# Optimization experiments

Hardware: AMD Instinct MI355X
Metric: run time of the kernel (lower is better)

## Reference

```python
import jax, jax.numpy as jnp
import numpy as np

N_NODES = 100000
N_EDGES = 1600000
D = 128
N_GRAPHS = 128
N_LAYERS = 3


def setup_inputs() -> dict:
    key = jax.random.key(0)
    ks = jax.random.split(key, 3 + 4 * N_LAYERS)
    x = jax.random.normal(ks[0], (N_NODES, D), dtype=jnp.float32)
    edge_index = jax.random.randint(ks[1], (2, N_EDGES), 0, N_NODES, dtype=jnp.int64)
    batch = jnp.sort(jax.random.randint(ks[2], (N_NODES,), 0, N_GRAPHS, dtype=jnp.int64))
    inp = {"x": x, "edge_index": edge_index, "batch": batch}
    scale = 1.0 / np.sqrt(D)
    for l in range(N_LAYERS):
        inp[f"W1_{l}"] = jax.random.normal(ks[3 + 4 * l], (D, D), dtype=jnp.float32) * scale
        inp[f"b1_{l}"] = jnp.zeros((D,), dtype=jnp.float32)
        inp[f"W2_{l}"] = jax.random.normal(ks[4 + 4 * l], (D, D), dtype=jnp.float32) * scale
        inp[f"b2_{l}"] = jnp.zeros((D,), dtype=jnp.float32)
    return inp


def _gin_conv(x, edge_index, W1, b1, W2, b2):
    # GINConv with eps=0: out = MLP(x + sum_{j in N(i)} x_j)
    msgs = x[edge_index[0]]                                   # [E, D] gather
    agg = jax.ops.segment_sum(msgs, edge_index[1], num_segments=N_NODES)
    h = x + agg
    h = jax.nn.relu(h @ W1 + b1)
    return h @ W2 + b2


def reference(x, edge_index, batch,
              W1_0, b1_0, W2_0, b2_0,
              W1_1, b1_1, W2_1, b2_1,
              W1_2, b1_2, W2_2, b2_2):
    params = [(W1_0, b1_0, W2_0, b2_0), (W1_1, b1_1, W2_1, b2_1), (W1_2, b1_2, W2_2, b2_2)]
    h = x
    for l in range(N_LAYERS - 1):
        h = _gin_conv(h, edge_index, *params[l])
        h = jax.nn.relu(h)  # act; dropout with drop_ratio=0 is identity
    node_emb = _gin_conv(h, edge_index, *params[-1])  # JK='last'
    # global_mean_pool
    sums = jax.ops.segment_sum(node_emb, batch, num_segments=N_GRAPHS)
    counts = jax.ops.segment_sum(jnp.ones((N_NODES, 1), node_emb.dtype), batch, num_segments=N_GRAPHS)
    graph_emb = sums / jnp.maximum(counts, 1.0)
    return graph_emb
```

## Files before the change

kernel.cpp:

```cpp
#include <hip/hip_runtime.h>
#include <hip/hip_bf16.h>

#define N_NODES 100000
#define N_PAD   100032
#define N_EDGES 1600000
#define DIM 128
#define N_GRAPHS 128
#define NBKT 98
#define BSTRIDE 18432
#define TILES (N_PAD / 16)
#define GRID_MLP 1563
#define POOL_BLKS ((N_NODES + 127) / 128)
#define B1_BATCH 4096
#define B1_GRID ((N_EDGES + B1_BATCH - 1) / B1_BATCH)

typedef unsigned short u16;
typedef unsigned int u32;
typedef __attribute__((ext_vector_type(8))) short bf16x8;
typedef __attribute__((ext_vector_type(4))) float f32x4;

#define MFMA(A, B, C) __builtin_amdgcn_mfma_f32_16x16x32_bf16(A, B, C, 0, 0, 0)

__device__ __forceinline__ u16 f2bf(float x) {
    u32 u = __float_as_uint(x);
    u = (u + 0x7FFFu + ((u >> 16) & 1u)) >> 16;
    return (u16)u;
}
__device__ __forceinline__ float bf2f(u16 u) {
    return __uint_as_float(((u32)u) << 16);
}

__global__ __launch_bounds__(256) void bucket1_kernel(const int* __restrict__ src,
                                                      const int* __restrict__ dst,
                                                      u32* __restrict__ cursorB,
                                                      u32* __restrict__ pairs) {
    __shared__ int lh[NBKT];
    __shared__ u32 lbase[NBKT];
    int t = threadIdx.x;
    if (t < NBKT) lh[t] = 0;
    __syncthreads();
    int e0 = blockIdx.x * B1_BATCH;
    int d[16], s[16], rk[16];
#pragma unroll
    for (int k = 0; k < 16; ++k) {
        int e = e0 + t + k * 256;
        if (e < N_EDGES) {
            d[k] = dst[e];
            s[k] = src[e];
            rk[k] = atomicAdd(&lh[d[k] >> 10], 1);
        }
    }
    __syncthreads();
    if (t < NBKT) lbase[t] = atomicAdd(&cursorB[t], (u32)lh[t]) + (u32)(t * BSTRIDE);
    __syncthreads();
#pragma unroll
    for (int k = 0; k < 16; ++k) {
        int e = e0 + t + k * 256;
        if (e < N_EDGES) {
            u32 pos = lbase[d[k] >> 10] + (u32)rk[k];
            pairs[pos] = ((u32)(d[k] & 1023) << 22) | (u32)s[k];
        }
    }
}

__global__ __launch_bounds__(1024) void bucket2_kernel(const u32* __restrict__ cursorB,
                                                       const u32* __restrict__ pairs,
                                                       int* __restrict__ row_ptr,
                                                       int* __restrict__ csr) {
    __shared__ int lh[1024];
    __shared__ int rc[1024];
    __shared__ int bs[128];
    int b = blockIdx.x, t = threadIdx.x;

    if (t < 128) bs[t] = (t < NBKT) ? (int)cursorB[t] : 0;
    __syncthreads();
    for (int off = 1; off < 128; off <<= 1) {
        int v = (t < 128 && t >= off) ? bs[t - off] : 0;
        __syncthreads();
        if (t < 128) bs[t] += v;
        __syncthreads();
    }
    int cnt = (int)cursorB[b];
    int bbase = (b == 0) ? 0 : bs[b - 1];

    lh[t] = 0;
    __syncthreads();
    const u32* pb = pairs + (size_t)b * BSTRIDE;
    for (int i = t; i < cnt; i += 1024) atomicAdd(&lh[__builtin_nontemporal_load(pb + i) >> 22], 1);
    __syncthreads();

    int own = lh[t];
    for (int off = 1; off < 1024; off <<= 1) {
        int v = (t >= off) ? lh[t - off] : 0;
        __syncthreads();
        lh[t] += v;
        __syncthreads();
    }
    int excl = lh[t] - own;
    int node = b * 1024 + t;
    if (node < N_NODES) row_ptr[node] = bbase + excl;
    if (b == 0 && t == 0) row_ptr[N_NODES] = N_EDGES;
    rc[t] = bbase + excl;
    __syncthreads();

    for (int i = t; i < cnt; i += 1024) {
        u32 p = __builtin_nontemporal_load(pb + i);
        int pos = atomicAdd(&rc[p >> 22], 1);
        csr[pos] = (int)(p & 0x3FFFFFu);
    }
}

__global__ __launch_bounds__(256) void xprep_kernel(const float* __restrict__ x,
                                                    u16* __restrict__ hb) {
    int i = blockIdx.x * 256 + threadIdx.x;
    if (i < N_NODES * 32) {
        float4 v = ((const float4*)x)[i];
        ushort4 o;
        o.x = f2bf(v.x); o.y = f2bf(v.y); o.z = f2bf(v.z); o.w = f2bf(v.w);
        ((ushort4*)hb)[i] = o;
    }
}

__global__ __launch_bounds__(256) void agg_kernel(const u16* __restrict__ hb,
                                                  const int* __restrict__ rp,
                                                  const int* __restrict__ csr,
                                                  u16* __restrict__ Ah) {
    int node = (blockIdx.x * 256 + threadIdx.x) >> 5;
    int l = threadIdx.x & 31;
    if (node >= N_NODES) return;
    const ushort4* h4 = (const ushort4*)hb;
    ushort4 sv = h4[(size_t)node * 32 + l];
    float a0 = bf2f(sv.x), a1 = bf2f(sv.y), a2 = bf2f(sv.z), a3 = bf2f(sv.w);
    int s = rp[node], e = rp[node + 1];
    int i = s;
    for (; i + 8 <= e; i += 8) {
        ushort4 v0 = h4[(size_t)csr[i + 0] * 32 + l];
        ushort4 v1 = h4[(size_t)csr[i + 1] * 32 + l];
        ushort4 v2 = h4[(size_t)csr[i + 2] * 32 + l];
        ushort4 v3 = h4[(size_t)csr[i + 3] * 32 + l];
        ushort4 v4 = h4[(size_t)csr[i + 4] * 32 + l];
        ushort4 v5 = h4[(size_t)csr[i + 5] * 32 + l];
        ushort4 v6 = h4[(size_t)csr[i + 6] * 32 + l];
        ushort4 v7 = h4[(size_t)csr[i + 7] * 32 + l];
        a0 += ((bf2f(v0.x) + bf2f(v1.x)) + (bf2f(v2.x) + bf2f(v3.x))) +
              ((bf2f(v4.x) + bf2f(v5.x)) + (bf2f(v6.x) + bf2f(v7.x)));
        a1 += ((bf2f(v0.y) + bf2f(v1.y)) + (bf2f(v2.y) + bf2f(v3.y))) +
              ((bf2f(v4.y) + bf2f(v5.y)) + (bf2f(v6.y) + bf2f(v7.y)));
        a2 += ((bf2f(v0.z) + bf2f(v1.z)) + (bf2f(v2.z) + bf2f(v3.z))) +
              ((bf2f(v4.z) + bf2f(v5.z)) + (bf2f(v6.z) + bf2f(v7.z)));
        a3 += ((bf2f(v0.w) + bf2f(v1.w)) + (bf2f(v2.w) + bf2f(v3.w))) +
              ((bf2f(v4.w) + bf2f(v5.w)) + (bf2f(v6.w) + bf2f(v7.w)));
    }
    for (; i < e; ++i) {
        ushort4 v = h4[(size_t)csr[i] * 32 + l];
        a0 += bf2f(v.x); a1 += bf2f(v.y); a2 += bf2f(v.z); a3 += bf2f(v.w);
    }
    ushort4 hv;
    hv.x = f2bf(a0); hv.y = f2bf(a1); hv.z = f2bf(a2); hv.w = f2bf(a3);
    *(ushort4*)(Ah + (size_t)node * 128 + l * 4) = hv;
}

struct WPrepArgs {
    const float* w[6];
    u16* buf[6];
};
__global__ __launch_bounds__(256) void wprep_kernel(WPrepArgs p) {
    int m = blockIdx.y;
    int idx = blockIdx.x * 256 + threadIdx.x;
    int n = idx >> 7, k = idx & 127;
    float v = p.w[m][k * 128 + n];
    u16 hi = f2bf(v);
    p.buf[m][idx] = hi;
    p.buf[m][idx + 16384] = f2bf(v - bf2f(hi));
}

#define HS 136
__global__ __launch_bounds__(256, 2) void fused_mlp(const u16* __restrict__ Ah,
                                                    const u16* __restrict__ W1,
                                                    const float* __restrict__ b1,
                                                    const u16* __restrict__ W2,
                                                    const float* __restrict__ b2,
                                                    u16* __restrict__ Cb, int relu) {
    __shared__ u16 Hh[64 * HS];
    __shared__ u16 Hl[64 * HS];
    int tid = threadIdx.x;
    int lane = tid & 63, wave = tid >> 6;
    int m16 = lane & 15, quad = lane >> 4;
    int colBase = wave * 32;

    float b1v[2][4], b2v[2][4];
#pragma unroll
    for (int nt = 0; nt < 2; ++nt)
#pragma unroll
        for (int rg = 0; rg < 4; ++rg) {
            int col = colBase + nt * 16 + quad * 4 + rg;
            b1v[nt][rg] = b1[col];
            b2v[nt][rg] = b2[col];
        }

    f32x4 z = {0.f, 0.f, 0.f, 0.f};
    bf16x8 aH[4][4];

    int t0 = blockIdx.x * 4;
    if (t0 >= TILES) return;
#pragma unroll
    for (int p = 0; p < 4; ++p) {
        const u16* ah = Ah + (size_t)((t0 + p) * 16 + m16) * 128 + quad * 8;
#pragma unroll
        for (int kb = 0; kb < 4; ++kb)
            aH[p][kb] = *(const bf16x8*)(ah + kb * 32);
    }

    bf16x8 W1H[2][4], W1L[2][4];
#pragma unroll
    for (int nt = 0; nt < 2; ++nt) {
        int n = colBase + nt * 16 + m16;
#pragma unroll
        for (int kb = 0; kb < 4; ++kb) {
            int off = n * 128 + kb * 32 + quad * 8;
            W1H[nt][kb] = *(const bf16x8*)(W1 + off);
            W1L[nt][kb] = *(const bf16x8*)(W1 + off + 16384);
        }
    }

    f32x4 acc[4][2];
#pragma unroll
    for (int p = 0; p < 4; ++p) { acc[p][0] = z; acc[p][1] = z; }

#pragma unroll
    for (int kb = 0; kb < 4; ++kb) {
#pragma unroll
        for (int p = 0; p < 4; ++p) {
            acc[p][0] = MFMA(W1H[0][kb], aH[p][kb], acc[p][0]);
            acc[p][1] = MFMA(W1H[1][kb], aH[p][kb], acc[p][1]);
            acc[p][0] = MFMA(W1L[0][kb], aH[p][kb], acc[p][0]);
            acc[p][1] = MFMA(W1L[1][kb], aH[p][kb], acc[p][1]);
        }
    }

#pragma unroll
    for (int p = 0; p < 4; ++p) {
#pragma unroll
        for (int nt = 0; nt < 2; ++nt) {
            ushort4 hv, lv;
#pragma unroll
            for (int rg = 0; rg < 4; ++rg) {
                float v = fmaxf(acc[p][nt][rg] + b1v[nt][rg], 0.f);
                u16 hi = f2bf(v);
                ((u16*)&hv)[rg] = hi;
                ((u16*)&lv)[rg] = f2bf(v - bf2f(hi));
            }
            int off = (p * 16 + m16) * HS + colBase + nt * 16 + quad * 4;
            *(ushort4*)&Hh[off] = hv;
            *(ushort4*)&Hl[off] = lv;
        }
    }
    __syncthreads();

    bf16x8 W2H[2][4], W2L[2][4];
#pragma unroll
    for (int nt = 0; nt < 2; ++nt) {
        int n = colBase + nt * 16 + m16;
#pragma unroll
        for (int kb = 0; kb < 4; ++kb) {
            int off = n * 128 + kb * 32 + quad * 8;
            W2H[nt][kb] = *(const bf16x8*)(W2 + off);
            W2L[nt][kb] = *(const bf16x8*)(W2 + off + 16384);
        }
    }

    f32x4 acc2[4][2];
#pragma unroll
    for (int p = 0; p < 4; ++p) { acc2[p][0] = z; acc2[p][1] = z; }
#pragma unroll
    for (int kb = 0; kb < 4; ++kb) {
#pragma unroll
        for (int p = 0; p < 4; ++p) {
            int off = (p * 16 + m16) * HS + kb * 32 + quad * 8;
            bf16x8 hH = *(const bf16x8*)(&Hh[off]);
            bf16x8 hL = *(const bf16x8*)(&Hl[off]);
            acc2[p][0] = MFMA(W2H[0][kb], hH, acc2[p][0]);
            acc2[p][1] = MFMA(W2H[1][kb], hH, acc2[p][1]);
            acc2[p][0] = MFMA(W2H[0][kb], hL, acc2[p][0]);
            acc2[p][1] = MFMA(W2H[1][kb], hL, acc2[p][1]);
            acc2[p][0] = MFMA(W2L[0][kb], hH, acc2[p][0]);
            acc2[p][1] = MFMA(W2L[1][kb], hH, acc2[p][1]);
        }
    }

#pragma unroll
    for (int p = 0; p < 4; ++p) {
        size_t row = (size_t)(t0 + p) * 16 + m16;
#pragma unroll
        for (int nt = 0; nt < 2; ++nt) {
            int col = colBase + nt * 16 + quad * 4;
            ushort4 o;
#pragma unroll
            for (int rg = 0; rg < 4; ++rg) {
                float v = acc2[p][nt][rg] + b2v[nt][rg];
                if (relu) v = fmaxf(v, 0.f);
                ((u16*)&o)[rg] = f2bf(v);
            }
            *(ushort4*)(Cb + row * 128 + col) = o;
        }
    }
}

__global__ __launch_bounds__(256) void psum_kernel(const u16* __restrict__ h,
                                                   const int* __restrict__ batch,
                                                   float* __restrict__ sums) {
    __shared__ int sBatch[128];
    int blk = blockIdx.x, t = threadIdx.x;
    int n0 = blk * 128;
    int nEnd = min(n0 + 128, N_NODES);
    if (t < 128 && n0 + t < N_NODES) sBatch[t] = batch[n0 + t];
    __syncthreads();

    int j = t & 127;
    int half = t >> 7;
    int s = n0 + half * 64;
    int e = min(s + 64, nEnd);

    float acc = 0.f;
    int cur = -1;
    for (int n = s; n < e; ++n) {
        int g = sBatch[n - n0];
        if (g != cur) {
            if (cur >= 0) atomicAdd(&sums[cur * 128 + j], acc);
            cur = g;
            acc = 0.f;
        }
        acc += bf2f(h[(size_t)n * 128 + j]);
    }
    if (cur >= 0) atomicAdd(&sums[cur * 128 + j], acc);
}

__global__ __launch_bounds__(128) void pdiv_kernel(const float* __restrict__ sums,
                                                   const int* __restrict__ batch,
                                                   float* __restrict__ out) {
    __shared__ int sB[2];
    int g = blockIdx.x;
    if (threadIdx.x < 2) {
        int target = g + threadIdx.x;
        int lo = 0, hi = N_NODES;
        while (lo < hi) {
            int m = (lo + hi) >> 1;
            if (batch[m] < target) lo = m + 1; else hi = m;
        }
        sB[threadIdx.x] = lo;
    }
    __syncthreads();
    float cnt = (float)(sB[1] - sB[0]);
    out[g * 128 + threadIdx.x] = sums[g * 128 + threadIdx.x] / fmaxf(cnt, 1.f);
}

extern "C" void kernel_launch(void* const* d_in, const int* in_sizes, int n_in,
                              void* d_out, int out_size, void* d_ws, size_t ws_size,
                              hipStream_t stream) {
    const float* x     = (const float*)d_in[0];
    const int*   ei    = (const int*)d_in[1];
    const int*   batch = (const int*)d_in[2];
    const int*   eSrc  = ei;
    const int*   eDst  = ei + N_EDGES;

    const float* W1[3] = {(const float*)d_in[3], (const float*)d_in[7],  (const float*)d_in[11]};
    const float* b1[3] = {(const float*)d_in[4], (const float*)d_in[8],  (const float*)d_in[12]};
    const float* W2[3] = {(const float*)d_in[5], (const float*)d_in[9],  (const float*)d_in[13]};
    const float* b2[3] = {(const float*)d_in[6], (const float*)d_in[10], (const float*)d_in[14]};

    float* P2 = (float*)d_ws;
    u16*   hb = (u16*)(P2 + (size_t)N_PAD * DIM);
    u16*   Ah = hb + (size_t)N_PAD * DIM;
    u16*   Wb = Ah + (size_t)N_PAD * DIM;
    int*   row_ptr = (int*)(Wb + 6 * 32768);
    u32*   cursorB = (u32*)(row_ptr + N_NODES + 8);
    int*   csr     = (int*)(cursorB + 128);
    float* sums    = (float*)(csr + N_EDGES);
    u32*   pairs   = (u32*)P2;

    hipMemsetAsync(cursorB, 0, 128 * sizeof(u32), stream);
    bucket1_kernel<<<B1_GRID, 256, 0, stream>>>(eSrc, eDst, cursorB, pairs);
    bucket2_kernel<<<NBKT, 1024, 0, stream>>>(cursorB, pairs, row_ptr, csr);

    xprep_kernel<<<(N_NODES * 32 + 255) / 256, 256, 0, stream>>>(x, hb);
    WPrepArgs wp;
    for (int l = 0; l < 3; ++l) {
        wp.w[2 * l]       = W1[l];
        wp.w[2 * l + 1]   = W2[l];
        wp.buf[2 * l]     = Wb + (size_t)(2 * l) * 32768;
        wp.buf[2 * l + 1] = Wb + (size_t)(2 * l + 1) * 32768;
    }
    wprep_kernel<<<dim3(64, 6), 256, 0, stream>>>(wp);
    hipMemsetAsync(sums, 0, N_GRAPHS * DIM * sizeof(float), stream);

    const int aggGrid = (N_NODES * 32 + 255) / 256;

    for (int l = 0; l < 3; ++l) {
        agg_kernel<<<aggGrid, 256, 0, stream>>>(hb, row_ptr, csr, Ah);
        fused_mlp<<<GRID_MLP, 256, 0, stream>>>(Ah,
                                                Wb + (size_t)(2 * l) * 32768, b1[l],
                                                Wb + (size_t)(2 * l + 1) * 32768, b2[l],
                                                hb, (l < 2) ? 1 : 0);
    }
    psum_kernel<<<POOL_BLKS, 256, 0, stream>>>(hb, batch, sums);
    pdiv_kernel<<<N_GRAPHS, 128, 0, stream>>>(sums, batch, (float*)d_out);
}
```

Measured before the change: 519.3 us.

## Fuse neighbor aggregation into the GIN MLP kernel with ping-pong buffers

Merges the separate CSR gather-sum kernel into the fused MLP kernel. Each block aggregates its 64 nodes into shared memory, then loads the MFMA A-operands from LDS instead of a global Ah buffer. Input and output features ping-pong between two planes, since a layer cannot overwrite its own input while other blocks still gather from it. This removes one launch per layer and the Ah round trip, but the irregular gather now runs inside a 2-blocks-per-SIMD MLP kernel with 16 lanes per node, which may hurt latency hiding.

Result: faster. 487.0 us (median of 2 runs) (-6.2%).

```diff
diff --git a/kernel.cpp b/kernel.cpp
--- a/kernel.cpp
+++ b/kernel.cpp
@@ -9,7 +9,7 @@
 #define NBKT 98
 #define BSTRIDE 18432
 #define TILES (N_PAD / 16)
-#define GRID_MLP 1563
+#define GRID_FUSED 1563
 #define POOL_BLKS ((N_NODES + 127) / 128)
 #define B1_BATCH 4096
 #define B1_GRID ((N_EDGES + B1_BATCH - 1) / B1_BATCH)
@@ -17,6 +17,7 @@
 typedef unsigned short u16;
 typedef unsigned int u32;
 typedef __attribute__((ext_vector_type(8))) short bf16x8;
+typedef __attribute__((ext_vector_type(8))) unsigned short u16x8;
 typedef __attribute__((ext_vector_type(4))) float f32x4;
 
 #define MFMA(A, B, C) __builtin_amdgcn_mfma_f32_16x16x32_bf16(A, B, C, 0, 0, 0)
@@ -119,45 +120,6 @@
         o.x = f2bf(v.x); o.y = f2bf(v.y); o.z = f2bf(v.z); o.w = f2bf(v.w);
         ((ushort4*)hb)[i] = o;
     }
-}
-
-__global__ __launch_bounds__(256) void agg_kernel(const u16* __restrict__ hb,
-                                                  const int* __restrict__ rp,
-                                                  const int* __restrict__ csr,
-                                                  u16* __restrict__ Ah) {
-    int node = (blockIdx.x * 256 + threadIdx.x) >> 5;
-    int l = threadIdx.x & 31;
-    if (node >= N_NODES) return;
-    const ushort4* h4 = (const ushort4*)hb;
-    ushort4 sv = h4[(size_t)node * 32 + l];
-    float a0 = bf2f(sv.x), a1 = bf2f(sv.y), a2 = bf2f(sv.z), a3 = bf2f(sv.w);
-    int s = rp[node], e = rp[node + 1];
-    int i = s;
-    for (; i + 8 <= e; i += 8) {
-        ushort4 v0 = h4[(size_t)csr[i + 0] * 32 + l];
-        ushort4 v1 = h4[(size_t)csr[i + 1] * 32 + l];
-        ushort4 v2 = h4[(size_t)csr[i + 2] * 32 + l];
-        ushort4 v3 = h4[(size_t)csr[i + 3] * 32 + l];
-        ushort4 v4 = h4[(size_t)csr[i + 4] * 32 + l];
-        ushort4 v5 = h4[(size_t)csr[i + 5] * 32 + l];
-        ushort4 v6 = h4[(size_t)csr[i + 6] * 32 + l];
-        ushort4 v7 = h4[(size_t)csr[i + 7] * 32 + l];
-        a0 += ((bf2f(v0.x) + bf2f(v1.x)) + (bf2f(v2.x) + bf2f(v3.x))) +
-              ((bf2f(v4.x) + bf2f(v5.x)) + (bf2f(v6.x) + bf2f(v7.x)));
-        a1 += ((bf2f(v0.y) + bf2f(v1.y)) + (bf2f(v2.y) + bf2f(v3.y))) +
-              ((bf2f(v4.y) + bf2f(v5.y)) + (bf2f(v6.y) + bf2f(v7.y)));
-        a2 += ((bf2f(v0.z) + bf2f(v1.z)) + (bf2f(v2.z) + bf2f(v3.z))) +
-              ((bf2f(v4.z) + bf2f(v5.z)) + (bf2f(v6.z) + bf2f(v7.z)));
-        a3 += ((bf2f(v0.w) + bf2f(v1.w)) + (bf2f(v2.w) + bf2f(v3.w))) +
-              ((bf2f(v4.w) + bf2f(v5.w)) + (bf2f(v6.w) + bf2f(v7.w)));
-    }
-    for (; i < e; ++i) {
-        ushort4 v = h4[(size_t)csr[i] * 32 + l];
-        a0 += bf2f(v.x); a1 += bf2f(v.y); a2 += bf2f(v.z); a3 += bf2f(v.w);
-    }
-    ushort4 hv;
-    hv.x = f2bf(a0); hv.y = f2bf(a1); hv.z = f2bf(a2); hv.w = f2bf(a3);
-    *(ushort4*)(Ah + (size_t)node * 128 + l * 4) = hv;
 }
 
 struct WPrepArgs {
@@ -175,18 +137,77 @@
 }
 
 #define HS 136
-__global__ __launch_bounds__(256, 2) void fused_mlp(const u16* __restrict__ Ah,
+__global__ __launch_bounds__(256, 2) void gin_layer(const u16* __restrict__ hin,
+                                                    const int* __restrict__ rp,
+                                                    const int* __restrict__ csr,
                                                     const u16* __restrict__ W1,
                                                     const float* __restrict__ b1,
                                                     const u16* __restrict__ W2,
                                                     const float* __restrict__ b2,
-                                                    u16* __restrict__ Cb, int relu) {
+                                                    u16* __restrict__ hout, int relu) {
     __shared__ u16 Hh[64 * HS];
     __shared__ u16 Hl[64 * HS];
     int tid = threadIdx.x;
     int lane = tid & 63, wave = tid >> 6;
     int m16 = lane & 15, quad = lane >> 4;
     int colBase = wave * 32;
+    int t0 = blockIdx.x * 4;
+    int r0 = t0 * 16;
+
+    {
+        int qw = tid >> 4;
+        int f  = tid & 15;
+        int nb = r0 + qw * 4;
+        const u16x8* h8 = (const u16x8*)hin;
+#pragma unroll
+        for (int j = 0; j < 4; ++j) {
+            int n = nb + j;
+            int nl = qw * 4 + j;
+            float a[8];
+            if (n < N_NODES) {
+                u16x8 sv = h8[(size_t)n * 16 + f];
+#pragma unroll
+                for (int r = 0; r < 8; ++r) a[r] = bf2f(sv[r]);
+                int s = rp[n], e = rp[n + 1];
+                int i = s;
+                for (; i + 8 <= e; i += 8) {
+                    u16x8 v0 = h8[(size_t)csr[i + 0] * 16 + f];
+                    u16x8 v1 = h8[(size_t)csr[i + 1] * 16 + f];
+                    u16x8 v2 = h8[(size_t)csr[i + 2] * 16 + f];
+                    u16x8 v3 = h8[(size_t)csr[i + 3] * 16 + f];
+                    u16x8 v4 = h8[(size_t)csr[i + 4] * 16 + f];
+                    u16x8 v5 = h8[(size_t)csr[i + 5] * 16 + f];
+                    u16x8 v6 = h8[(size_t)csr[i + 6] * 16 + f];
+                    u16x8 v7 = h8[(size_t)csr[i + 7] * 16 + f];
+#pragma unroll
+                    for (int r = 0; r < 8; ++r)
+                        a[r] += ((bf2f(v0[r]) + bf2f(v1[r])) + (bf2f(v2[r]) + bf2f(v3[r]))) +
+                                ((bf2f(v4[r]) + bf2f(v5[r])) + (bf2f(v6[r]) + bf2f(v7[r])));
+                }
+                for (; i < e; ++i) {
+                    u16x8 v = h8[(size_t)csr[i] * 16 + f];
+#pragma unroll
+                    for (int r = 0; r < 8; ++r) a[r] += bf2f(v[r]);
+                }
+            } else {
+#pragma unroll
+                for (int r = 0; r < 8; ++r) a[r] = 0.f;
+            }
+            u16x8 o;
+#pragma unroll
+            for (int r = 0; r < 8; ++r) o[r] = f2bf(a[r]);
+            *(u16x8*)&Hh[nl * HS + f * 8] = o;
+        }
+    }
+    __syncthreads();
+
+    bf16x8 aH[4][4];
+#pragma unroll
+    for (int p = 0; p < 4; ++p)
+#pragma unroll
+        for (int kb = 0; kb < 4; ++kb)
+            aH[p][kb] = *(const bf16x8*)&Hh[(p * 16 + m16) * HS + kb * 32 + quad * 8];
+    __syncthreads();
 
     float b1v[2][4], b2v[2][4];
 #pragma unroll
@@ -199,17 +220,6 @@
         }
 
     f32x4 z = {0.f, 0.f, 0.f, 0.f};
-    bf16x8 aH[4][4];
-
-    int t0 = blockIdx.x * 4;
-    if (t0 >= TILES) return;
-#pragma unroll
-    for (int p = 0; p < 4; ++p) {
-        const u16* ah = Ah + (size_t)((t0 + p) * 16 + m16) * 128 + quad * 8;
-#pragma unroll
-        for (int kb = 0; kb < 4; ++kb)
-            aH[p][kb] = *(const bf16x8*)(ah + kb * 32);
-    }
 
     bf16x8 W1H[2][4], W1L[2][4];
 #pragma unroll
@@ -301,7 +311,7 @@
                 if (relu) v = fmaxf(v, 0.f);
                 ((u16*)&o)[rg] = f2bf(v);
             }
-            *(ushort4*)(Cb + row * 128 + col) = o;
+            *(ushort4*)(hout + row * 128 + col) = o;
         }
     }
 }
@@ -369,8 +379,9 @@
     const float* b2[3] = {(const float*)d_in[6], (const float*)d_in[10], (const float*)d_in[14]};
 
     float* P2 = (float*)d_ws;
-    u16*   hb = (u16*)(P2 + (size_t)N_PAD * DIM);
-    u16*   Ah = hb + (size_t)N_PAD * DIM;
+    u16*   planeB = (u16*)P2;
+    u16*   planeA = (u16*)(P2 + (size_t)N_PAD * DIM);
+    u16*   Ah = planeA + (size_t)N_PAD * DIM;
     u16*   Wb = Ah + (size_t)N_PAD * DIM;
     int*   row_ptr = (int*)(Wb + 6 * 32768);
     u32*   cursorB = (u32*)(row_ptr + N_NODES + 8);
@@ -382,7 +393,7 @@
     bucket1_kernel<<<B1_GRID, 256, 0, stream>>>(eSrc, eDst, cursorB, pairs);
     bucket2_kernel<<<NBKT, 1024, 0, stream>>>(cursorB, pairs, row_ptr, csr);
 
-    xprep_kernel<<<(N_NODES * 32 + 255) / 256, 256, 0, stream>>>(x, hb);
+    xprep_kernel<<<(N_NODES * 32 + 255) / 256, 256, 0, stream>>>(x, planeA);
     WPrepArgs wp;
     for (int l = 0; l < 3; ++l) {
         wp.w[2 * l]       = W1[l];
@@ -393,15 +404,15 @@
     wprep_kernel<<<dim3(64, 6), 256, 0, stream>>>(wp);
     hipMemsetAsync(sums, 0, N_GRAPHS * DIM * sizeof(float), stream);
 
-    const int aggGrid = (N_NODES * 32 + 255) / 256;
-
+    u16* hin  = planeA;
+    u16* hout = planeB;
     for (int l = 0; l < 3; ++l) {
-        agg_kernel<<<aggGrid, 256, 0, stream>>>(hb, row_ptr, csr, Ah);
-        fused_mlp<<<GRID_MLP, 256, 0, stream>>>(Ah,
-                                                Wb + (size_t)(2 * l) * 32768, b1[l],
-                                                Wb + (size_t)(2 * l + 1) * 32768, b2[l],
-                                                hb, (l < 2) ? 1 : 0);
-    }
-    psum_kernel<<<POOL_BLKS, 256, 0, stream>>>(hb, batch, sums);
+        gin_layer<<<GRID_FUSED, 256, 0, stream>>>(hin, row_ptr, csr,
+                                                  Wb + (size_t)(2 * l) * 32768, b1[l],
+                                                  Wb + (size_t)(2 * l + 1) * 32768, b2[l],
+                                                  hout, (l < 2) ? 1 : 0);
+        u16* tmp = hin; hin = hout; hout = tmp;
+    }
+    psum_kernel<<<POOL_BLKS, 256, 0, stream>>>(hin, batch, sums);
     pdiv_kernel<<<N_GRAPHS, 128, 0, stream>>>(sums, batch, (float*)d_out);
 }
```
